# Optimization experiments

Measured on AMD Instinct MI355X. Metric: run time of the kernel, lower is better.

The kernel has to match this reference:

```python
import jax, jax.numpy as jnp
import numpy as np

B = 32768      # batch
H = 256        # num_heads
Q = 4          # n_qubits_per_head == d_k (seq_len=1 forced by module's reshape)
E = H * Q      # embed_dim = 1024


def setup_inputs() -> dict:
    key = jax.random.key(0)
    k1, k2, k3 = jax.random.split(key, 3)
    x = jax.random.normal(k1, (B, 1, E), dtype=jnp.float32)
    # trainable RX angles, one per (head, qubit)
    theta = jax.random.normal(k2, (H, Q), dtype=jnp.float32) * 0.1
    # combine Linear params
    W = jax.random.normal(k3, (E, E), dtype=jnp.float32) / np.float32(np.sqrt(E))
    b = jnp.zeros((E,), dtype=jnp.float32)
    return {"x": x, "theta": theta, "W": W, "b": b}


def reference(x, theta, W, b):
    # x: (B, 1, E). Split into heads: view(B, S=1, H, Q) -> head i input flattened to (B, Q)
    Bn, S, En = x.shape
    Hn, Qn = theta.shape
    hx = x.reshape(Bn, Hn, Qn)                      # (B, H, Q), S == 1
    # Quantum circuit per head: RX(x) then RX(theta) on each wire of |0>^Q.
    # RX(a)RX(b) = RX(a+b); product state => <Z_i> = cos(x_i + theta_i)
    z = jnp.cos(hx + theta[None, :, :])             # (B, H, Q)
    # torch: stack over heads (B,H,Q) -> transpose(1,2) -> (B,Q,H) -> view(B,1,E)
    out = jnp.transpose(z, (0, 2, 1)).reshape(Bn, 1, En)
    # dropout in eval mode = identity; combine Linear
    return out @ W.T + b
```

## Files before the change

kernel.cpp:

```cpp
#include <hip/hip_runtime.h>
#include <hip/hip_bf16.h>


typedef unsigned short u16;
typedef __attribute__((ext_vector_type(8))) short bf16x8;
typedef __attribute__((ext_vector_type(8))) unsigned short u16x8;
typedef __attribute__((ext_vector_type(4))) float f32x4;

#define NB   32768
#define EDIM 1024
#define KK   1024
#define BM   256
#define BN   256
#define BK   64
#define NT   48

__device__ inline u16 f2bf(float f) {
  unsigned u = __float_as_uint(f);
  return (u16)((u + 0x7fffu + ((u >> 16) & 1u)) >> 16);
}
__device__ inline float bf2f(u16 h) { return __uint_as_float((unsigned)h << 16); }

__device__ inline void gload_lds16(const void* g, void* l) {
  __builtin_amdgcn_global_load_lds(
      (const __attribute__((address_space(1))) unsigned int*)g,
      (__attribute__((address_space(3))) unsigned int*)l, 16, 0, 0);
}

__global__ __launch_bounds__(256) void qmha_act(
    const float* __restrict__ x, const float* __restrict__ theta,
    u16* __restrict__ a_hi, u16* __restrict__ a_lo) {
  const int nthreads = gridDim.x * 256;
  const int total8 = NB * KK / 8;
  for (int v = blockIdx.x * 256 + threadIdx.x; v < total8; v += nthreads) {
    const float4 x0 = ((const float4*)x)[2 * v];
    const float4 x1 = ((const float4*)x)[2 * v + 1];
    const float4 t0 = ((const float4*)theta)[(2 * v) & 255];
    const float4 t1 = ((const float4*)theta)[(2 * v + 1) & 255];
    const float s[8] = {x0.x + t0.x, x0.y + t0.y, x0.z + t0.z, x0.w + t0.w,
                        x1.x + t1.x, x1.y + t1.y, x1.z + t1.z, x1.w + t1.w};
    u16x8 h, l;
#pragma unroll
    for (int j = 0; j < 8; ++j) {
      float z = __builtin_amdgcn_cosf(
          __builtin_amdgcn_fractf(s[j] * 0.15915494309189535f));
      u16 hh = f2bf(z);
      h[j] = hh;
      l[j] = f2bf(z - bf2f(hh));
    }
    ((u16x8*)a_hi)[v] = h;
    ((u16x8*)a_lo)[v] = l;
  }
}

__global__ __launch_bounds__(256) void qmha_wsplit(
    const float* __restrict__ W, u16* __restrict__ w_hi, u16* __restrict__ w_lo) {
  const int i4 = blockIdx.x * 256 + threadIdx.x;
  const int e  = i4 >> 8;
  const int jb = i4 & 255;
  const float* wrow = W + (size_t)e * 1024;
  ushort4 h, l;
  u16* hp = &h.x;
  u16* lp = &l.x;
#pragma unroll
  for (int jj = 0; jj < 4; ++jj) {
    const float wv = wrow[jj * 256 + jb];
    u16 hh = f2bf(wv);
    hp[jj] = hh;
    lp[jj] = f2bf(wv - bf2f(hh));
  }
  ((ushort4*)w_hi)[i4] = h;
  ((ushort4*)w_lo)[i4] = l;
}


#define LOADA(S, QM)                                                         \
  {                                                                          \
    const int arow0 = wm * 128 + ((QM) ^ wm) * 64 + lrow;                    \
    _Pragma("unroll")                                                        \
    for (int mi = 0; mi < 4; ++mi)                                           \
      _Pragma("unroll")                                                      \
      for (int ks = 0; ks < 2; ++ks)                                         \
        af[mi][ks] = *(const bf16x8*)&As[S][(arow0 + mi * 16) * 64 +         \
            (((ks * 4 + lk) ^ (lrow & 7)) << 3)];                            \
  }

#define LOADB(S, QN, BF)                                                     \
  {                                                                          \
    const int brow0 = wn * 64 + ((QN) ^ (wn & 1)) * 32 + lrow;               \
    _Pragma("unroll")                                                        \
    for (int ni = 0; ni < 2; ++ni)                                           \
      _Pragma("unroll")                                                      \
      for (int ks = 0; ks < 2; ++ks)                                         \
        BF[ni][ks] = *(const bf16x8*)&Bs[S][(brow0 + ni * 16) * 64 +         \
            (((ks * 4 + lk) ^ (lrow & 7)) << 3)];                            \
  }

#define MFMA_PHASE(QM, QN, BF, TAIL)                                         \
  __builtin_amdgcn_s_barrier();                                              \
  asm volatile("s_waitcnt lgkmcnt(0)" ::: "memory");                         \
  __builtin_amdgcn_sched_barrier(0);                                         \
  __builtin_amdgcn_s_setprio(1);                                             \
  _Pragma("unroll")                                                          \
  for (int ks = 0; ks < 2; ++ks)                                             \
    _Pragma("unroll")                                                        \
    for (int mi = 0; mi < 4; ++mi)                                           \
      _Pragma("unroll")                                                      \
      for (int ni = 0; ni < 2; ++ni)                                         \
        acc[(QM) * 4 + mi][(QN) * 2 + ni] =                                  \
            __builtin_amdgcn_mfma_f32_16x16x32_bf16(                         \
                af[mi][ks], BF[ni][ks],                                      \
                acc[(QM) * 4 + mi][(QN) * 2 + ni], 0, 0, 0);                 \
  __builtin_amdgcn_s_setprio(0);                                             \
  TAIL;                                                                      \
  __builtin_amdgcn_s_barrier();

#define GROUP(S, G, VMWAIT)                                                  \
  {                                                                          \
    bf16x8 af[4][2], bf0[2][2], bf1[2][2];                                   \
    LOADA(S, 0)                                                              \
    LOADB(S, 0, bf0)                                                         \
    stageA(1 - (S), (G) + 1, 1);                                             \
    stageA(1 - (S), (G) + 1, 2);                                             \
    MFMA_PHASE(0, 0, bf0, )                                                  \
    LOADB(S, 1, bf1)                                                         \
    stageB(1 - (S), (G) + 1, 0);                                             \
    stageB(1 - (S), (G) + 1, 1);                                             \
    MFMA_PHASE(0, 1, bf1, )                                                  \
    LOADA(S, 1)                                                              \
    stageB(1 - (S), (G) + 1, 2);                                             \
    stageB(1 - (S), (G) + 1, 3);                                             \
    MFMA_PHASE(1, 0, bf0, )                                                  \
    stageA((S), (G) + 2, 0);                                                 \
    stageA((S), (G) + 2, 3);                                                 \
    MFMA_PHASE(1, 1, bf1,                                                    \
               asm volatile("s_waitcnt " VMWAIT ::: "memory"))               \
  }

__global__ __launch_bounds__(512, 2) void qmha_gemm(
    const u16* __restrict__ a_hi, const u16* __restrict__ a_lo,
    const u16* __restrict__ w_hi, const u16* __restrict__ w_lo,
    const float* __restrict__ bias, float* __restrict__ out) {
  __shared__ __align__(16) u16 As[2][BM * BK];
  __shared__ __align__(16) u16 Bs[2][BN * BK];

  const int tid  = threadIdx.x;
  const int lane = tid & 63;
  const int wave = tid >> 6;
  const int wm = wave >> 2;
  const int wn = wave & 3;
  const int lrow = lane & 15;
  const int lk   = lane >> 4;

  const int bid = blockIdx.x;
  const int r   = bid >> 3;
  const int bm  = ((bid & 7) * 16 + (r & 15)) * BM;
  const int bn  = (r >> 4) * BN;

  auto Aptr = [&](int t) -> const u16* { return (t & 16) ? a_lo : a_hi; };
  auto Bptr = [&](int t) -> const u16* { return (t >= 32) ? w_lo : w_hi; };

  const int srow8 = (tid >> 3) & 7;
  const int scol  = ((tid & 7) ^ srow8) * 8;
  const int ldst  = (tid >> 6) * 512;

  auto stageA = [&](int s, int t, int q) {
    if (t >= NT) return;
    const u16* A = Aptr(t);
    const int k0 = (t & 15) * BK;
    const int row = bm + q * 64 + (tid >> 3);
    gload_lds16(A + (size_t)row * KK + (k0 + scol), &As[s][q * 4096 + ldst]);
  };
  auto stageB = [&](int s, int t, int q) {
    if (t >= NT) return;
    const u16* Bp = Bptr(t);
    const int k0 = (t & 15) * BK;
    const int row = bn + q * 64 + (tid >> 3);
    gload_lds16(Bp + (size_t)row * KK + (k0 + scol), &Bs[s][q * 4096 + ldst]);
  };

  f32x4 acc[8][4];
#pragma unroll
  for (int i = 0; i < 8; ++i)
#pragma unroll
    for (int j = 0; j < 4; ++j) acc[i][j] = f32x4{0.f, 0.f, 0.f, 0.f};

#pragma unroll
  for (int q = 0; q < 4; ++q) {
    stageA(0, 0, q);
    stageB(0, 0, q);
  }
  stageA(1, 1, 0);
  stageA(1, 1, 3);
  asm volatile("s_waitcnt vmcnt(2)" ::: "memory");
  __builtin_amdgcn_s_barrier();

  for (int g = 0; g < NT - 2; g += 2) {
    GROUP(0, g, "vmcnt(2)")
    GROUP(1, g + 1, "vmcnt(2)")
  }
  GROUP(0, NT - 2, "vmcnt(0)")
  GROUP(1, NT - 1, "vmcnt(0)")

#pragma unroll
  for (int qm = 0; qm < 2; ++qm)
#pragma unroll
    for (int mi = 0; mi < 4; ++mi) {
      const int row0 = bm + wm * 128 + (qm ^ wm) * 64 + mi * 16 + lk * 4;
#pragma unroll
      for (int qn = 0; qn < 2; ++qn)
#pragma unroll
        for (int ni = 0; ni < 2; ++ni) {
          const int col = bn + wn * 64 + (qn ^ (wn & 1)) * 32 + ni * 16 + lrow;
          const float bv = bias[col];
          const f32x4 a = acc[qm * 4 + mi][qn * 2 + ni];
#pragma unroll
          for (int rr = 0; rr < 4; ++rr)
            out[(size_t)(row0 + rr) * EDIM + col] = a[rr] + bv;
        }
    }
}

extern "C" void kernel_launch(void* const* d_in, const int* in_sizes, int n_in,
                              void* d_out, int out_size, void* d_ws, size_t ws_size,
                              hipStream_t stream) {
  (void)in_sizes; (void)n_in; (void)out_size; (void)ws_size;
  const float* x     = (const float*)d_in[0];
  const float* theta = (const float*)d_in[1];
  const float* W     = (const float*)d_in[2];
  const float* b     = (const float*)d_in[3];
  float* out = (float*)d_out;

  unsigned char* ws = (unsigned char*)d_ws;
  u16* a_hi = (u16*)(ws);
  u16* a_lo = (u16*)(ws + (size_t)NB * KK * 2);
  u16* w_hi = (u16*)(ws + (size_t)NB * KK * 4);
  u16* w_lo = (u16*)(ws + (size_t)NB * KK * 4 + (size_t)EDIM * KK * 2);

  qmha_act<<<2048, 256, 0, stream>>>(x, theta, a_hi, a_lo);
  qmha_wsplit<<<1024, 256, 0, stream>>>(W, w_hi, w_lo);
  qmha_gemm<<<(NB / BM) * (EDIM / BN), 512, 0, stream>>>(a_hi, a_lo, w_hi, w_lo,
                                                         b, out);
}
```

Before: 422.0 us.

## Fuse cosine activation into GEMM and drop bf16x3 split for single fp16 MFMA

Replaces the split-bf16 hi/lo GEMM, which ran 48 K-tiles (hi*hi, lo*hi, hi*lo), with a single fp16 GEMM of 16 K-tiles. The cosine activation is now computed inside the GEMM: raw x is loaded to registers, cos is applied, and the fp16 result is written to swizzled LDS. This removes the separate activation kernel and its large workspace round trip. In exchange, accuracy drops to fp16 inputs, and the A tile pays register pressure and VALU work plus a full vmcnt(0) wait each tile.

```diff
diff --git a/kernel.cpp b/kernel.cpp
--- a/kernel.cpp
+++ b/kernel.cpp
@@ -3,8 +3,7 @@
 
 
 typedef unsigned short u16;
-typedef __attribute__((ext_vector_type(8))) short bf16x8;
-typedef __attribute__((ext_vector_type(8))) unsigned short u16x8;
+typedef __attribute__((ext_vector_type(8))) _Float16 f16x8;
 typedef __attribute__((ext_vector_type(4))) float f32x4;
 
 #define NB   32768
@@ -13,13 +12,7 @@
 #define BM   256
 #define BN   256
 #define BK   64
-#define NT   48
-
-__device__ inline u16 f2bf(float f) {
-  unsigned u = __float_as_uint(f);
-  return (u16)((u + 0x7fffu + ((u >> 16) & 1u)) >> 16);
-}
-__device__ inline float bf2f(u16 h) { return __uint_as_float((unsigned)h << 16); }
+#define NT   16
 
 __device__ inline void gload_lds16(const void* g, void* l) {
   __builtin_amdgcn_global_load_lds(
@@ -27,50 +20,22 @@
       (__attribute__((address_space(3))) unsigned int*)l, 16, 0, 0);
 }
 
-__global__ __launch_bounds__(256) void qmha_act(
-    const float* __restrict__ x, const float* __restrict__ theta,
-    u16* __restrict__ a_hi, u16* __restrict__ a_lo) {
-  const int nthreads = gridDim.x * 256;
-  const int total8 = NB * KK / 8;
-  for (int v = blockIdx.x * 256 + threadIdx.x; v < total8; v += nthreads) {
-    const float4 x0 = ((const float4*)x)[2 * v];
-    const float4 x1 = ((const float4*)x)[2 * v + 1];
-    const float4 t0 = ((const float4*)theta)[(2 * v) & 255];
-    const float4 t1 = ((const float4*)theta)[(2 * v + 1) & 255];
-    const float s[8] = {x0.x + t0.x, x0.y + t0.y, x0.z + t0.z, x0.w + t0.w,
-                        x1.x + t1.x, x1.y + t1.y, x1.z + t1.z, x1.w + t1.w};
-    u16x8 h, l;
-#pragma unroll
-    for (int j = 0; j < 8; ++j) {
-      float z = __builtin_amdgcn_cosf(
-          __builtin_amdgcn_fractf(s[j] * 0.15915494309189535f));
-      u16 hh = f2bf(z);
-      h[j] = hh;
-      l[j] = f2bf(z - bf2f(hh));
-    }
-    ((u16x8*)a_hi)[v] = h;
-    ((u16x8*)a_lo)[v] = l;
-  }
-}
-
-__global__ __launch_bounds__(256) void qmha_wsplit(
-    const float* __restrict__ W, u16* __restrict__ w_hi, u16* __restrict__ w_lo) {
+__device__ inline _Float16 qcos(float s) {
+  return (_Float16)__builtin_amdgcn_cosf(
+      __builtin_amdgcn_fractf(s * 0.15915494309189535f));
+}
+
+__global__ __launch_bounds__(256) void qmha_wprep(
+    const float* __restrict__ W, _Float16* __restrict__ w16) {
   const int i4 = blockIdx.x * 256 + threadIdx.x;
   const int e  = i4 >> 8;
   const int jb = i4 & 255;
   const float* wrow = W + (size_t)e * 1024;
-  ushort4 h, l;
-  u16* hp = &h.x;
-  u16* lp = &l.x;
-#pragma unroll
-  for (int jj = 0; jj < 4; ++jj) {
-    const float wv = wrow[jj * 256 + jb];
-    u16 hh = f2bf(wv);
-    hp[jj] = hh;
-    lp[jj] = f2bf(wv - bf2f(hh));
-  }
-  ((ushort4*)w_hi)[i4] = h;
-  ((ushort4*)w_lo)[i4] = l;
+  union { _Float16 h[4]; uint2 u; } P;
+#pragma unroll
+  for (int jj = 0; jj < 4; ++jj)
+    P.h[jj] = (_Float16)wrow[jj * 256 + jb];
+  ((uint2*)w16)[i4] = P.u;
 }
 
 
@@ -81,7 +46,7 @@
     for (int mi = 0; mi < 4; ++mi)                                           \
       _Pragma("unroll")                                                      \
       for (int ks = 0; ks < 2; ++ks)                                         \
-        af[mi][ks] = *(const bf16x8*)&As[S][(arow0 + mi * 16) * 64 +         \
+        af[mi][ks] = *(const f16x8*)&As[S][(arow0 + mi * 16) * 64 +          \
             (((ks * 4 + lk) ^ (lrow & 7)) << 3)];                            \
   }
 
@@ -92,7 +57,7 @@
     for (int ni = 0; ni < 2; ++ni)                                           \
       _Pragma("unroll")                                                      \
       for (int ks = 0; ks < 2; ++ks)                                         \
-        BF[ni][ks] = *(const bf16x8*)&Bs[S][(brow0 + ni * 16) * 64 +         \
+        BF[ni][ks] = *(const f16x8*)&Bs[S][(brow0 + ni * 16) * 64 +          \
             (((ks * 4 + lk) ^ (lrow & 7)) << 3)];                            \
   }
 
@@ -108,41 +73,42 @@
       _Pragma("unroll")                                                      \
       for (int ni = 0; ni < 2; ++ni)                                         \
         acc[(QM) * 4 + mi][(QN) * 2 + ni] =                                  \
-            __builtin_amdgcn_mfma_f32_16x16x32_bf16(                         \
+            __builtin_amdgcn_mfma_f32_16x16x32_f16(                          \
                 af[mi][ks], BF[ni][ks],                                      \
                 acc[(QM) * 4 + mi][(QN) * 2 + ni], 0, 0, 0);                 \
   __builtin_amdgcn_s_setprio(0);                                             \
   TAIL;                                                                      \
   __builtin_amdgcn_s_barrier();
 
-#define GROUP(S, G, VMWAIT)                                                  \
+#define GROUP(S, T, PF)                                                      \
   {                                                                          \
-    bf16x8 af[4][2], bf0[2][2], bf1[2][2];                                   \
+    f16x8 af[4][2], bf0[2][2], bf1[2][2];                                    \
     LOADA(S, 0)                                                              \
     LOADB(S, 0, bf0)                                                         \
-    stageA(1 - (S), (G) + 1, 1);                                             \
-    stageA(1 - (S), (G) + 1, 2);                                             \
+    if (PF) {                                                                \
+      stageB(1 - (S), (T) + 1, 0);                                           \
+      stageB(1 - (S), (T) + 1, 1);                                           \
+      issueA((T) + 1);                                                       \
+    }                                                                        \
     MFMA_PHASE(0, 0, bf0, )                                                  \
     LOADB(S, 1, bf1)                                                         \
-    stageB(1 - (S), (G) + 1, 0);                                             \
-    stageB(1 - (S), (G) + 1, 1);                                             \
+    if (PF) {                                                                \
+      stageB(1 - (S), (T) + 1, 2);                                           \
+      stageB(1 - (S), (T) + 1, 3);                                           \
+    }                                                                        \
     MFMA_PHASE(0, 1, bf1, )                                                  \
     LOADA(S, 1)                                                              \
-    stageB(1 - (S), (G) + 1, 2);                                             \
-    stageB(1 - (S), (G) + 1, 3);                                             \
-    MFMA_PHASE(1, 0, bf0, )                                                  \
-    stageA((S), (G) + 2, 0);                                                 \
-    stageA((S), (G) + 2, 3);                                                 \
+    MFMA_PHASE(1, 0, bf0, if (PF) { cvtWriteA(1 - (S)); })                   \
     MFMA_PHASE(1, 1, bf1,                                                    \
-               asm volatile("s_waitcnt " VMWAIT ::: "memory"))               \
+               asm volatile("s_waitcnt vmcnt(0)" ::: "memory"))              \
   }
 
 __global__ __launch_bounds__(512, 2) void qmha_gemm(
-    const u16* __restrict__ a_hi, const u16* __restrict__ a_lo,
-    const u16* __restrict__ w_hi, const u16* __restrict__ w_lo,
-    const float* __restrict__ bias, float* __restrict__ out) {
-  __shared__ __align__(16) u16 As[2][BM * BK];
-  __shared__ __align__(16) u16 Bs[2][BN * BK];
+    const float* __restrict__ x, const float* __restrict__ theta,
+    const _Float16* __restrict__ w16, const float* __restrict__ bias,
+    float* __restrict__ out) {
+  __shared__ __align__(16) _Float16 As[2][BM * BK];
+  __shared__ __align__(16) _Float16 Bs[2][BN * BK];
 
   const int tid  = threadIdx.x;
   const int lane = tid & 63;
@@ -157,27 +123,38 @@
   const int bm  = ((bid & 7) * 16 + (r & 15)) * BM;
   const int bn  = (r >> 4) * BN;
 
-  auto Aptr = [&](int t) -> const u16* { return (t & 16) ? a_lo : a_hi; };
-  auto Bptr = [&](int t) -> const u16* { return (t >= 32) ? w_lo : w_hi; };
-
   const int srow8 = (tid >> 3) & 7;
   const int scol  = ((tid & 7) ^ srow8) * 8;
-  const int ldst  = (tid >> 6) * 512;
-
-  auto stageA = [&](int s, int t, int q) {
-    if (t >= NT) return;
-    const u16* A = Aptr(t);
-    const int k0 = (t & 15) * BK;
-    const int row = bm + q * 64 + (tid >> 3);
-    gload_lds16(A + (size_t)row * KK + (k0 + scol), &As[s][q * 4096 + ldst]);
+  const int ldst  = wave * 512;
+  auto stageB = [&](int s, int t, int q) {
+    const int row = bn + q * 64 + (tid >> 3);
+    gload_lds16(w16 + (size_t)row * KK + (t * BK + scol), &Bs[s][q * 4096 + ldst]);
   };
-  auto stageB = [&](int s, int t, int q) {
-    if (t >= NT) return;
-    const u16* Bp = Bptr(t);
-    const int k0 = (t & 15) * BK;
-    const int row = bn + q * 64 + (tid >> 3);
-    gload_lds16(Bp + (size_t)row * KK + (k0 + scol), &Bs[s][q * 4096 + ldst]);
+
+  float4 xr[8];
+  float4 tv;
+  const int ar0 = tid >> 4;
+  const int hc  = tid & 15;
+  auto issueA = [&](int t) {
+    const float* xp = x + (size_t)(bm + ar0) * KK + t * BK + hc * 4;
+#pragma unroll
+    for (int u = 0; u < 8; ++u)
+      xr[u] = *(const float4*)(xp + (size_t)u * 32 * KK);
+    tv = *(const float4*)(theta + t * BK + hc * 4);
   };
+  auto cvtWriteA = [&](int s) {
+#pragma unroll
+    for (int u = 0; u < 8; ++u) {
+      const int rr = u * 32 + ar0;
+      union { _Float16 h[4]; uint2 uu; } P;
+      P.h[0] = qcos(xr[u].x + tv.x);
+      P.h[1] = qcos(xr[u].y + tv.y);
+      P.h[2] = qcos(xr[u].z + tv.z);
+      P.h[3] = qcos(xr[u].w + tv.w);
+      const int sc = (hc >> 1) ^ (rr & 7);
+      *(uint2*)&As[s][rr * 64 + sc * 8 + (hc & 1) * 4] = P.uu;
+    }
+  };
 
   f32x4 acc[8][4];
 #pragma unroll
@@ -186,21 +163,18 @@
     for (int j = 0; j < 4; ++j) acc[i][j] = f32x4{0.f, 0.f, 0.f, 0.f};
 
 #pragma unroll
-  for (int q = 0; q < 4; ++q) {
-    stageA(0, 0, q);
-    stageB(0, 0, q);
-  }
-  stageA(1, 1, 0);
-  stageA(1, 1, 3);
-  asm volatile("s_waitcnt vmcnt(2)" ::: "memory");
+  for (int q = 0; q < 4; ++q) stageB(0, 0, q);
+  issueA(0);
+  cvtWriteA(0);
+  asm volatile("s_waitcnt vmcnt(0) lgkmcnt(0)" ::: "memory");
   __builtin_amdgcn_s_barrier();
 
   for (int g = 0; g < NT - 2; g += 2) {
-    GROUP(0, g, "vmcnt(2)")
-    GROUP(1, g + 1, "vmcnt(2)")
-  }
-  GROUP(0, NT - 2, "vmcnt(0)")
-  GROUP(1, NT - 1, "vmcnt(0)")
+    GROUP(0, g, 1)
+    GROUP(1, g + 1, 1)
+  }
+  GROUP(0, NT - 2, 1)
+  GROUP(1, NT - 1, 0)
 
 #pragma unroll
   for (int qm = 0; qm < 2; ++qm)
@@ -231,14 +205,8 @@
   const float* b     = (const float*)d_in[3];
   float* out = (float*)d_out;
 
-  unsigned char* ws = (unsigned char*)d_ws;
-  u16* a_hi = (u16*)(ws);
-  u16* a_lo = (u16*)(ws + (size_t)NB * KK * 2);
-  u16* w_hi = (u16*)(ws + (size_t)NB * KK * 4);
-  u16* w_lo = (u16*)(ws + (size_t)NB * KK * 4 + (size_t)EDIM * KK * 2);
-
-  qmha_act<<<2048, 256, 0, stream>>>(x, theta, a_hi, a_lo);
-  qmha_wsplit<<<1024, 256, 0, stream>>>(W, w_hi, w_lo);
-  qmha_gemm<<<(NB / BM) * (EDIM / BN), 512, 0, stream>>>(a_hi, a_lo, w_hi, w_lo,
-                                                         b, out);
-}
+  _Float16* w16 = (_Float16*)d_ws;
+
+  qmha_wprep<<<1024, 256, 0, stream>>>(W, w16);
+  qmha_gemm<<<(NB / BM) * (EDIM / BN), 512, 0, stream>>>(x, theta, w16, b, out);
+}
```

New measurement: 362.7 us. 14.0% less time.
